# Kernel tuning notes

Hardware: AMD Instinct MI355X
Metric: run time of the kernel (lower is better)

The kernel has to match this reference:

```python
import jax, jax.numpy as jnp
import numpy as np

D_IN, D_OUT, RANK = 4096, 4096, 16
ALPHA = 1.0


def setup_inputs() -> dict:
    key = jax.random.key(0)
    ks = jax.random.split(key, 7)
    x = jax.random.normal(ks[0], (8, 2048, D_IN), dtype=jnp.float32)
    W = jax.random.normal(ks[1], (D_IN, D_OUT), dtype=jnp.float32) * (1.0 / np.sqrt(D_IN))
    bias = jax.random.normal(ks[2], (D_OUT,), dtype=jnp.float32) * 0.02
    # he_normal init for a factors; b factors are zeros in the layer, but use small
    # random values so the adapter path contributes numerically to the test.
    a0 = jax.random.normal(ks[3], (D_IN, RANK), dtype=jnp.float32) * np.sqrt(2.0 / D_IN)
    b0 = jax.random.normal(ks[4], (RANK, D_OUT), dtype=jnp.float32) * 0.02
    a1 = jax.random.normal(ks[5], (D_IN, RANK), dtype=jnp.float32) * np.sqrt(2.0 / D_IN)
    b1 = jax.random.normal(ks[6], (RANK, D_OUT), dtype=jnp.float32) * 0.02
    return {"x": x, "W": W, "bias": bias, "a0": a0, "b0": b0, "a1": a1, "b1": b1}


def reference(x, W, bias, a0, b0, a1, b1):
    # LoHA kernel: base + Hadamard product of scaled low-rank factors
    scale = ALPHA / RANK
    p0 = scale * (a0 @ b0)            # [d_in, d_out]
    p1 = scale * (a1 @ b1)            # [d_in, d_out]
    kernel = W + p0 * p1              # [d_in, d_out]
    # Dense call: x @ kernel + bias
    return jnp.einsum('bsd,de->bse', x, kernel) + bias
```

## Files before the change

kernel.cpp:

```cpp
#include <hip/hip_runtime.h>


#define D_IN   4096
#define D_OUT  4096
#define RANKR  16
#define MROWS  16384
#define NTILES 64

typedef __attribute__((ext_vector_type(8))) short short8;
typedef __attribute__((ext_vector_type(4))) float floatx4;

__device__ __forceinline__ unsigned short f2bf(float f) {
    union { float f; unsigned u; } c; c.f = f;
    unsigned r = c.u + 0x7fffu + ((c.u >> 16) & 1u);
    return (unsigned short)(r >> 16);
}

__device__ __forceinline__ void glds16(const void* g, void* l) {
    __builtin_amdgcn_global_load_lds(
        (const __attribute__((address_space(1))) void*)g,
        (__attribute__((address_space(3))) void*)l, 16, 0, 0);
}

__global__ __launch_bounds__(256) void cvt_x(const float* __restrict__ x,
                                             unsigned short* __restrict__ xb) {
    size_t i = ((size_t)blockIdx.x * 256 + threadIdx.x) * 8;
    const float4* p = (const float4*)(x + i);
    float4 v0 = p[0], v1 = p[1];
    union { unsigned short u[8]; uint4 q; } o;
    o.u[0] = f2bf(v0.x); o.u[1] = f2bf(v0.y);
    o.u[2] = f2bf(v0.z); o.u[3] = f2bf(v0.w);
    o.u[4] = f2bf(v1.x); o.u[5] = f2bf(v1.y);
    o.u[6] = f2bf(v1.z); o.u[7] = f2bf(v1.w);
    *(uint4*)(xb + i) = o.q;
}

__global__ __launch_bounds__(256) void prep_bt(
    const float* __restrict__ W,  const float* __restrict__ a0,
    const float* __restrict__ b0, const float* __restrict__ a1,
    const float* __restrict__ b1, unsigned short* __restrict__ Bt) {
    __shared__ float Wt[64][65];
    __shared__ float b0t[64][20], b1t[64][20];
    const int tid = threadIdx.x;
    const int k0 = (blockIdx.x & 63) * 64, n0 = (blockIdx.x >> 6) * 64;

    #pragma unroll
    for (int i = 0; i < 16; ++i) {
        int e = i * 256 + tid;
        int kk = e >> 6, nn = e & 63;
        Wt[kk][nn] = W[(size_t)(k0 + kk) * D_OUT + n0 + nn];
    }
    #pragma unroll
    for (int i = 0; i < 4; ++i) {
        int e = i * 256 + tid;
        int r = e >> 6, nn = e & 63;
        b0t[nn][r] = b0[(size_t)r * D_OUT + n0 + nn];
        b1t[nn][r] = b1[(size_t)r * D_OUT + n0 + nn];
    }
    const int kk = tid & 63;
    float4 A0[4], A1[4];
    #pragma unroll
    for (int c = 0; c < 4; ++c) {
        A0[c] = *(const float4*)(a0 + (size_t)(k0 + kk) * RANKR + c * 4);
        A1[c] = *(const float4*)(a1 + (size_t)(k0 + kk) * RANKR + c * 4);
    }
    __syncthreads();

    const float s2 = 1.0f / 256.0f;
    #pragma unroll
    for (int i = 0; i < 16; ++i) {
        int nn = i * 4 + (tid >> 6);
        float d0 = 0.f, d1 = 0.f;
        #pragma unroll
        for (int c = 0; c < 4; ++c) {
            float4 bv0 = *(const float4*)&b0t[nn][c * 4];
            float4 bv1 = *(const float4*)&b1t[nn][c * 4];
            d0 += A0[c].x * bv0.x + A0[c].y * bv0.y + A0[c].z * bv0.z + A0[c].w * bv0.w;
            d1 += A1[c].x * bv1.x + A1[c].y * bv1.y + A1[c].z * bv1.z + A1[c].w * bv1.w;
        }
        float v = Wt[kk][nn] + s2 * d0 * d1;
        Bt[(size_t)(n0 + nn) * D_IN + k0 + kk] = f2bf(v);
    }
}

#define BAR do { asm volatile("" ::: "memory");                  \
                 __builtin_amdgcn_s_barrier();                   \
                 asm volatile("" ::: "memory"); } while (0)
#define VMC(N) asm volatile("s_waitcnt vmcnt(" #N ")" ::: "memory")
#define LGKM0  asm volatile("s_waitcnt lgkmcnt(0)" ::: "memory")

#define STG_A(NB, KK, KTN) do {                                               \
    glds16(Ag + gof0 + (KTN) + (KK) * 32, (char*)&As[NB][KK][0] + ldw0);      \
    glds16(Ag + gof1 + (KTN) + (KK) * 32, (char*)&As[NB][KK][0] + ldw1);      \
  } while (0)
#define STG_B(NB, KK, KTN) do {                                               \
    glds16(Bg + gof0 + (KTN) + (KK) * 32, (char*)&Bs[NB][KK][0] + ldw0);      \
    glds16(Bg + gof1 + (KTN) + (KK) * 32, (char*)&Bs[NB][KK][0] + ldw1);      \
  } while (0)

#define RD(DST, SRC, ROWB) _Pragma("unroll")                                  \
    for (int i_ = 0; i_ < 4; ++i_)                                            \
      DST[i_] = *(const short8*)(&SRC[((ROWB) + i_ * 16) * 32 + rc8]);

#define MM(AO, AF, BF) do {                                                   \
    __builtin_amdgcn_s_setprio(1);                                            \
    _Pragma("unroll")                                                         \
    for (int i_ = 0; i_ < 4; ++i_)                                            \
      _Pragma("unroll")                                                       \
      for (int j_ = 0; j_ < 4; ++j_)                                          \
        acc[(AO) + i_][j_] = __builtin_amdgcn_mfma_f32_16x16x32_bf16(         \
            AF[i_], BF[j_], acc[(AO) + i_][j_], 0, 0, 0);                     \
    __builtin_amdgcn_s_setprio(0);                                            \
  } while (0)

#define TILE(T, BUF) do {                                                     \
    const int ktn_ = ((T) + 1) * 64;                                          \
     RD(a0k0, As[BUF][0], arow); RD(b0, Bs[BUF][0], brow);              \
           STG_A(!(BUF), 0, ktn_);                                            \
           BAR; LGKM0; MM(4, a1k1, b1); BAR;                                  \
     RD(a1k0, As[BUF][0], arow + 64);                                   \
           STG_B(!(BUF), 0, ktn_); VMC(4);                                    \
           BAR; LGKM0; MM(0, a0k0, b0); BAR;                                  \
     RD(a0k1, As[BUF][1], arow); RD(b1, Bs[BUF][1], brow);              \
           STG_A(!(BUF), 1, ktn_);                                            \
           BAR; LGKM0; MM(4, a1k0, b0); BAR;                                  \
     RD(a1k1, As[BUF][1], arow + 64);                                   \
           STG_B(!(BUF), 1, ktn_); VMC(4);                                    \
           BAR; LGKM0; MM(0, a0k1, b1); BAR;                                  \
  } while (0)

__global__ __launch_bounds__(512, 2) void gemm_bt(
    const unsigned short* __restrict__ A,
    const unsigned short* __restrict__ B,
    const float* __restrict__ bias,
    float* __restrict__ C) {
    __shared__ __align__(16) unsigned short As[2][2][8192];
    __shared__ __align__(16) unsigned short Bs[2][2][8192];

    const int tid  = threadIdx.x;
    const int wave = tid >> 6, lane = tid & 63;
    const int quad = lane >> 4, l16 = lane & 15;
    const int rc8 = (quad ^ ((l16 >> 1) & 3)) * 8;

    const int bid = blockIdx.y * 16 + blockIdx.x;
    const int swz = (bid & 7) * 128 + (bid >> 3);
    const int m0 = (swz >> 4) * 256, n0 = (swz & 15) * 256;
    const int wm = wave >> 2, wn = wave & 3;
    const int arow = wm * 128 + l16;
    const int brow = wn * 64 + l16;

    const unsigned short* Ag = A + (size_t)m0 * D_IN;
    const unsigned short* Bg = B + (size_t)n0 * D_IN;

    const int e0 = tid, e1 = 512 + tid;
    const size_t gof0 = (size_t)(e0 >> 2) * D_IN + (size_t)(((e0 & 3) ^ ((e0 >> 3) & 3)) * 8);
    const size_t gof1 = (size_t)(e1 >> 2) * D_IN + (size_t)(((e1 & 3) ^ ((e1 >> 3) & 3)) * 8);
    const unsigned ldw0 = wave * 1024;
    const unsigned ldw1 = 8192 + wave * 1024;

    short8 a0k0[4], a1k0[4], a0k1[4], a1k1[4], b0[4], b1[4];
    floatx4 acc[8][4] = {};

    STG_A(0, 0, 0); STG_B(0, 0, 0); STG_A(0, 1, 0); STG_B(0, 1, 0);
    STG_A(1, 0, 64); STG_B(1, 0, 64);
    VMC(8);
    BAR;

     RD(a0k0, As[0][0], arow); RD(b0, Bs[0][0], brow); BAR;
     RD(a1k0, As[0][0], arow + 64); VMC(4);
           BAR; LGKM0; MM(0, a0k0, b0); BAR;
     RD(a0k1, As[0][1], arow); RD(b1, Bs[0][1], brow);
           STG_A(1, 1, 64);
           BAR; LGKM0; MM(4, a1k0, b0); BAR;
     RD(a1k1, As[0][1], arow + 64);
           STG_B(1, 1, 64); VMC(4);
           BAR; LGKM0; MM(0, a0k1, b1); BAR;

    for (int t = 1; t < NTILES - 2; t += 2) {
        TILE(t, 1);
        TILE(t + 1, 0);
    }

     RD(a0k0, As[1][0], arow); RD(b0, Bs[1][0], brow);
           BAR; LGKM0; MM(4, a1k1, b1); BAR;
     RD(a1k0, As[1][0], arow + 64); VMC(0);
           BAR; LGKM0; MM(0, a0k0, b0); BAR;
     RD(a0k1, As[1][1], arow); RD(b1, Bs[1][1], brow);
           BAR; LGKM0; MM(4, a1k0, b0); BAR;
     RD(a1k1, As[1][1], arow + 64);
           BAR; LGKM0; MM(0, a0k1, b1); BAR;
     MM(4, a1k1, b1);

    #pragma unroll
    for (int nt = 0; nt < 4; ++nt) {
        int col = n0 + wn * 64 + nt * 16 + l16;
        float bv = bias[col];
        #pragma unroll
        for (int mt = 0; mt < 8; ++mt) {
            int r0 = m0 + wm * 128 + mt * 16 + quad * 4;
            #pragma unroll
            for (int r = 0; r < 4; ++r) {
                float v = acc[mt][nt][r] + bv;
                __builtin_nontemporal_store(v, &C[(size_t)(r0 + r) * D_OUT + col]);
            }
        }
    }
}

extern "C" void kernel_launch(void* const* d_in, const int* in_sizes, int n_in,
                              void* d_out, int out_size, void* d_ws, size_t ws_size,
                              hipStream_t stream) {
    const float* x    = (const float*)d_in[0];
    const float* W    = (const float*)d_in[1];
    const float* bias = (const float*)d_in[2];
    const float* a0   = (const float*)d_in[3];
    const float* b0   = (const float*)d_in[4];
    const float* a1   = (const float*)d_in[5];
    const float* b1   = (const float*)d_in[6];
    float* out = (float*)d_out;

    unsigned short* xb = (unsigned short*)d_ws;
    unsigned short* Bt = (unsigned short*)((char*)d_ws + (size_t)MROWS * D_IN * 2);

    cvt_x<<<(MROWS * (size_t)D_IN) / 2048, 256, 0, stream>>>(x, xb);
    prep_bt<<<4096, 256, 0, stream>>>(W, a0, b0, a1, b1, Bt);
    gemm_bt<<<dim3(D_OUT / 256, MROWS / 256), 512, 0, stream>>>(xb, Bt, bias, out);
}
```

Before: 1.003 ms.

## Merge prep kernels and simplify GEMM main loop to two phases per tile

Combines the x bf16 conversion and the LoHA weight-prep into one launch, with a block-index split and nontemporal loads, to remove one kernel launch and its tail. The GEMM main loop is restructured so each K-tile runs in two phases (k-halves) that each load A and B fragments, issue both global-to-LDS stages, then run two MFMA groups between fewer barriers. This replaces the finer-grained four-phase interleave, trading fewer barriers and larger MFMA bursts for less overlap of LDS reads with MFMA work. It also holds more fragment registers live at once.

After: 955.3 us. 1.05x faster.

```diff
diff --git a/kernel.cpp b/kernel.cpp
--- a/kernel.cpp
+++ b/kernel.cpp
@@ -6,9 +6,11 @@
 #define RANKR  16
 #define MROWS  16384
 #define NTILES 64
+#define NCVT   32768
 
 typedef __attribute__((ext_vector_type(8))) short short8;
 typedef __attribute__((ext_vector_type(4))) float floatx4;
+typedef __attribute__((ext_vector_type(4))) unsigned int uintx4;
 
 __device__ __forceinline__ unsigned short f2bf(float f) {
     union { float f; unsigned u; } c; c.f = f;
@@ -22,33 +24,36 @@
         (__attribute__((address_space(3))) void*)l, 16, 0, 0);
 }
 
-__global__ __launch_bounds__(256) void cvt_x(const float* __restrict__ x,
-                                             unsigned short* __restrict__ xb) {
-    size_t i = ((size_t)blockIdx.x * 256 + threadIdx.x) * 8;
-    const float4* p = (const float4*)(x + i);
-    float4 v0 = p[0], v1 = p[1];
-    union { unsigned short u[8]; uint4 q; } o;
-    o.u[0] = f2bf(v0.x); o.u[1] = f2bf(v0.y);
-    o.u[2] = f2bf(v0.z); o.u[3] = f2bf(v0.w);
-    o.u[4] = f2bf(v1.x); o.u[5] = f2bf(v1.y);
-    o.u[6] = f2bf(v1.z); o.u[7] = f2bf(v1.w);
-    *(uint4*)(xb + i) = o.q;
-}
-
-__global__ __launch_bounds__(256) void prep_bt(
+__global__ __launch_bounds__(256) void prep(
     const float* __restrict__ W,  const float* __restrict__ a0,
     const float* __restrict__ b0, const float* __restrict__ a1,
-    const float* __restrict__ b1, unsigned short* __restrict__ Bt) {
+    const float* __restrict__ b1, unsigned short* __restrict__ Bt,
+    const float* __restrict__ x,  unsigned short* __restrict__ xb) {
+    const int tid = threadIdx.x;
+    if (blockIdx.x < NCVT) {
+        size_t i = ((size_t)blockIdx.x * 256 + tid) * 8;
+        const floatx4* p = (const floatx4*)(x + i);
+        floatx4 v0 = __builtin_nontemporal_load(p);
+        floatx4 v1 = __builtin_nontemporal_load(p + 1);
+        union { unsigned short u[8]; uintx4 q; } o;
+        o.u[0] = f2bf(v0.x); o.u[1] = f2bf(v0.y);
+        o.u[2] = f2bf(v0.z); o.u[3] = f2bf(v0.w);
+        o.u[4] = f2bf(v1.x); o.u[5] = f2bf(v1.y);
+        o.u[6] = f2bf(v1.z); o.u[7] = f2bf(v1.w);
+        *(uintx4*)(xb + i) = o.q;
+        return;
+    }
     __shared__ float Wt[64][65];
     __shared__ float b0t[64][20], b1t[64][20];
-    const int tid = threadIdx.x;
-    const int k0 = (blockIdx.x & 63) * 64, n0 = (blockIdx.x >> 6) * 64;
+    const int pb = blockIdx.x - NCVT;
+    const int k0 = (pb & 63) * 64, n0 = (pb >> 6) * 64;
 
     #pragma unroll
     for (int i = 0; i < 16; ++i) {
         int e = i * 256 + tid;
         int kk = e >> 6, nn = e & 63;
-        Wt[kk][nn] = W[(size_t)(k0 + kk) * D_OUT + n0 + nn];
+        Wt[kk][nn] = __builtin_nontemporal_load(
+            W + (size_t)(k0 + kk) * D_OUT + n0 + nn);
     }
     #pragma unroll
     for (int i = 0; i < 4; ++i) {
@@ -58,11 +63,11 @@
         b1t[nn][r] = b1[(size_t)r * D_OUT + n0 + nn];
     }
     const int kk = tid & 63;
-    float4 A0[4], A1[4];
+    floatx4 A0[4], A1[4];
     #pragma unroll
     for (int c = 0; c < 4; ++c) {
-        A0[c] = *(const float4*)(a0 + (size_t)(k0 + kk) * RANKR + c * 4);
-        A1[c] = *(const float4*)(a1 + (size_t)(k0 + kk) * RANKR + c * 4);
+        A0[c] = *(const floatx4*)(a0 + (size_t)(k0 + kk) * RANKR + c * 4);
+        A1[c] = *(const floatx4*)(a1 + (size_t)(k0 + kk) * RANKR + c * 4);
     }
     __syncthreads();
 
@@ -73,8 +78,8 @@
         float d0 = 0.f, d1 = 0.f;
         #pragma unroll
         for (int c = 0; c < 4; ++c) {
-            float4 bv0 = *(const float4*)&b0t[nn][c * 4];
-            float4 bv1 = *(const float4*)&b1t[nn][c * 4];
+            floatx4 bv0 = *(const floatx4*)&b0t[nn][c * 4];
+            floatx4 bv1 = *(const floatx4*)&b1t[nn][c * 4];
             d0 += A0[c].x * bv0.x + A0[c].y * bv0.y + A0[c].z * bv0.z + A0[c].w * bv0.w;
             d1 += A1[c].x * bv1.x + A1[c].y * bv1.y + A1[c].z * bv1.z + A1[c].w * bv1.w;
         }
@@ -113,20 +118,20 @@
     __builtin_amdgcn_s_setprio(0);                                            \
   } while (0)
 
-#define TILE(T, BUF) do {                                                     \
+#define TILE2(T, BUF) do {                                                    \
     const int ktn_ = ((T) + 1) * 64;                                          \
-     RD(a0k0, As[BUF][0], arow); RD(b0, Bs[BUF][0], brow);              \
-           STG_A(!(BUF), 0, ktn_);                                            \
-           BAR; LGKM0; MM(4, a1k1, b1); BAR;                                  \
-     RD(a1k0, As[BUF][0], arow + 64);                                   \
-           STG_B(!(BUF), 0, ktn_); VMC(4);                                    \
-           BAR; LGKM0; MM(0, a0k0, b0); BAR;                                  \
-     RD(a0k1, As[BUF][1], arow); RD(b1, Bs[BUF][1], brow);              \
-           STG_A(!(BUF), 1, ktn_);                                            \
-           BAR; LGKM0; MM(4, a1k0, b0); BAR;                                  \
-     RD(a1k1, As[BUF][1], arow + 64);                                   \
-           STG_B(!(BUF), 1, ktn_); VMC(4);                                    \
-           BAR; LGKM0; MM(0, a0k1, b1); BAR;                                  \
+     RD(af0, As[BUF][0], arow); RD(af1, As[BUF][0], arow + 64);        \
+            RD(bf0, Bs[BUF][0], brow);                                        \
+            STG_A(!(BUF), 0, ktn_); STG_B(!(BUF), 0, ktn_);                   \
+            VMC(4); BAR; LGKM0;                                               \
+            MM(0, af0, bf0); MM(4, af1, bf0);                                 \
+            BAR;                                                              \
+     RD(ag0, As[BUF][1], arow); RD(ag1, As[BUF][1], arow + 64);        \
+            RD(bf1, Bs[BUF][1], brow);                                        \
+            STG_A(!(BUF), 1, ktn_); STG_B(!(BUF), 1, ktn_);                   \
+            VMC(4); BAR; LGKM0;                                               \
+            MM(0, ag0, bf1); MM(4, ag1, bf1);                                 \
+            BAR;                                                              \
   } while (0)
 
 __global__ __launch_bounds__(512, 2) void gemm_bt(
@@ -158,38 +163,29 @@
     const unsigned ldw0 = wave * 1024;
     const unsigned ldw1 = 8192 + wave * 1024;
 
-    short8 a0k0[4], a1k0[4], a0k1[4], a1k1[4], b0[4], b1[4];
+    short8 af0[4], af1[4], ag0[4], ag1[4], bf0[4], bf1[4];
     floatx4 acc[8][4] = {};
 
-    STG_A(0, 0, 0); STG_B(0, 0, 0); STG_A(0, 1, 0); STG_B(0, 1, 0);
-    STG_A(1, 0, 64); STG_B(1, 0, 64);
-    VMC(8);
+    STG_A(0, 0, 0); STG_B(0, 0, 0);
+    STG_A(0, 1, 0); STG_B(0, 1, 0);
+    VMC(4);
     BAR;
 
-     RD(a0k0, As[0][0], arow); RD(b0, Bs[0][0], brow); BAR;
-     RD(a1k0, As[0][0], arow + 64); VMC(4);
-           BAR; LGKM0; MM(0, a0k0, b0); BAR;
-     RD(a0k1, As[0][1], arow); RD(b1, Bs[0][1], brow);
-           STG_A(1, 1, 64);
-           BAR; LGKM0; MM(4, a1k0, b0); BAR;
-     RD(a1k1, As[0][1], arow + 64);
-           STG_B(1, 1, 64); VMC(4);
-           BAR; LGKM0; MM(0, a0k1, b1); BAR;
-
-    for (int t = 1; t < NTILES - 2; t += 2) {
-        TILE(t, 1);
-        TILE(t + 1, 0);
-    }
-
-     RD(a0k0, As[1][0], arow); RD(b0, Bs[1][0], brow);
-           BAR; LGKM0; MM(4, a1k1, b1); BAR;
-     RD(a1k0, As[1][0], arow + 64); VMC(0);
-           BAR; LGKM0; MM(0, a0k0, b0); BAR;
-     RD(a0k1, As[1][1], arow); RD(b1, Bs[1][1], brow);
-           BAR; LGKM0; MM(4, a1k0, b0); BAR;
-     RD(a1k1, As[1][1], arow + 64);
-           BAR; LGKM0; MM(0, a0k1, b1); BAR;
-     MM(4, a1k1, b1);
+    for (int t = 0; t < NTILES - 2; t += 2) {
+        TILE2(t, 0);
+        TILE2(t + 1, 1);
+    }
+    TILE2(NTILES - 2, 0);
+
+     RD(af0, As[1][0], arow); RD(af1, As[1][0], arow + 64);
+            RD(bf0, Bs[1][0], brow);
+            VMC(0); BAR; LGKM0;
+            MM(0, af0, bf0); MM(4, af1, bf0);
+            BAR;
+     RD(ag0, As[1][1], arow); RD(ag1, As[1][1], arow + 64);
+            RD(bf1, Bs[1][1], brow);
+            LGKM0;
+            MM(0, ag0, bf1); MM(4, ag1, bf1);
 
     #pragma unroll
     for (int nt = 0; nt < 4; ++nt) {
@@ -222,7 +218,6 @@
     unsigned short* xb = (unsigned short*)d_ws;
     unsigned short* Bt = (unsigned short*)((char*)d_ws + (size_t)MROWS * D_IN * 2);
 
-    cvt_x<<<(MROWS * (size_t)D_IN) / 2048, 256, 0, stream>>>(x, xb);
-    prep_bt<<<4096, 256, 0, stream>>>(W, a0, b0, a1, b1, Bt);
+    prep<<<NCVT + 4096, 256, 0, stream>>>(W, a0, b0, a1, b1, Bt, x, xb);
     gemm_bt<<<dim3(D_OUT / 256, MROWS / 256), 512, 0, stream>>>(xb, Bt, bias, out);
 }
```
